# Performance work log

Hardware: AMD Instinct MI355X
Metric: run time of the kernel (lower is better)

The kernel has to match this reference:

```python
import jax, jax.numpy as jnp
import numpy as np

IN_DIM = 4096
OUT_DIM = 4096
CODEBOOK_SIZE = 65536
LAYER_ID = 3
HASH_A, HASH_B, HASH_C = 10007, 20011, 40009
SIGN_HASH_A, SIGN_HASH_B, SIGN_HASH_C = 4099, 6151, 14887
SIGNED_HASH = True
BATCH = 8192


def _hash_tables():
    i = jnp.arange(OUT_DIM, dtype=jnp.int64 if jax.config.jax_enable_x64 else jnp.int32)[:, None]
    j = jnp.arange(IN_DIM, dtype=i.dtype)[None, :]
    idx = (i * HASH_A + j * HASH_B + LAYER_ID * HASH_C) % CODEBOOK_SIZE
    bits = (i * SIGN_HASH_A + j * SIGN_HASH_B + LAYER_ID * SIGN_HASH_C) % 2
    signs = bits.astype(jnp.float32) * 2.0 - 1.0
    return idx, signs


def setup_inputs() -> dict:
    key = jax.random.key(0)
    kx, kc = jax.random.split(key)
    x = jax.random.normal(kx, (BATCH, IN_DIM), dtype=jnp.float32)
    codebook = jax.random.normal(kc, (CODEBOOK_SIZE,), dtype=jnp.float32) * 0.01
    bias = jnp.zeros((OUT_DIM,), dtype=jnp.float32)
    return {"x": x, "codebook": codebook, "bias": bias}


def reference(x, codebook, bias):
    idx, signs = _hash_tables()  # [out_dim, in_dim] each
    weight = codebook[idx]  # gather from tiny codebook -> [out_dim, in_dim]
    if SIGNED_HASH:
        weight = weight * signs.astype(weight.dtype)
    # F.linear: y = x @ W^T + b
    return jnp.einsum('bi,oi->bo', x, weight) + bias
```

## Files before the change

kernel.cpp:

```cpp
#include <hip/hip_runtime.h>
#include <hip/hip_bf16.h>

constexpr int M_ = 8192;
constexpr int N_ = 4096;
constexpr int K_ = 4096;
constexpr int CBOOK = 65536;
constexpr int HA = 10007, HB = 20011;
constexpr int HC3 = 3 * 40009;

constexpr int C0 = 197;

constexpr int BM = 256, BN = 256, BK = 32;
constexpr int NKT = K_ / BK;

using bf16x8 = __bf16 __attribute__((ext_vector_type(8)));
using f32x4  = float __attribute__((ext_vector_type(4)));
using u16x8  = unsigned short __attribute__((ext_vector_type(8)));

typedef __attribute__((address_space(3))) void lds_void_t;
typedef const __attribute__((address_space(1))) void gbl_void_t;

static __device__ __forceinline__ unsigned short f2bf(float f) {
    __bf16 h = (__bf16)f;
    return __builtin_bit_cast(unsigned short, h);
}

constexpr int P2N   = 8 * 65536;
constexpr int P2B   = P2N / 256;

__global__ __launch_bounds__(256) void prep_p2(const float* __restrict__ cb,
                                               unsigned short* __restrict__ P2p) {
    const int t = blockIdx.x * 256 + threadIdx.x;
    const int p = t >> 16;
    const int i = t & 65535;
    const int u = i + p;
    float v = cb[(u * HB + HC3) & (CBOOK - 1)];
    if (u & 1) v = -v;
    P2p[t] = f2bf(v);
}

constexpr int GENB  = N_ * K_ / 8 / 256;
constexpr int CONVB = M_ * K_ / 8 / 256;

__global__ __launch_bounds__(256) void prep_main(const float* __restrict__ x,
                                                 const unsigned short* __restrict__ P2p,
                                                 unsigned short* __restrict__ Wf,
                                                 unsigned short* __restrict__ xb) {
    const int b = blockIdx.x;
    if (b < GENB) {
        const int t    = b * 256 + threadIdx.x;
        const int slot = t & 1023;
        const int kt   = (t >> 10) & 127;
        const int nb   = t >> 17;
        const int row  = slot >> 2;
        const int key  = (row >> 1) & 3;
        const int n  = (nb << 8) + row;
        const int k0 = (kt << 5) + (((slot & 3) ^ key) << 3);
        const int u0 = (C0 * n + k0) & (CBOOK - 1);
        const u16x8 w = *reinterpret_cast<const u16x8*>(
            P2p + ((u0 & 7) << 16) + (u0 & 65528));
        *reinterpret_cast<u16x8*>(&Wf[(size_t)t * 8]) = w;
    } else {
        const size_t t = (size_t)(b - GENB) * 256 + threadIdx.x;
        const float4* p = reinterpret_cast<const float4*>(x) + t * 2;
        const float4 a = p[0], c = p[1];
        u16x8 out;
        out[0] = f2bf(a.x); out[1] = f2bf(a.y); out[2] = f2bf(a.z); out[3] = f2bf(a.w);
        out[4] = f2bf(c.x); out[5] = f2bf(c.y); out[6] = f2bf(c.z); out[7] = f2bf(c.w);
        reinterpret_cast<u16x8*>(xb)[t] = out;
    }
}

__global__ __launch_bounds__(512, 2) void gemm_kernel(
        const unsigned short* __restrict__ A,
        const unsigned short* __restrict__ Wf,
        const float* __restrict__ bias,
        float* __restrict__ C) {
    __shared__ __align__(16) unsigned short sm[3 * 8192 * 2];
    unsigned short* As = sm;
    unsigned short* Bs = sm + 3 * 8192;

    const int tid  = threadIdx.x;
    const int lane = tid & 63;
    const int w    = tid >> 6;
    const int wm   = w >> 2;
    const int wn   = w & 3;
    const int m0 = blockIdx.y * BM;
    const int n0 = blockIdx.x * BN;

    const int quad = lane >> 4;
    const int l16  = lane & 15;

    const int sblk = (lane & 3) ^ ((lane >> 3) & 3);
    const unsigned short* aLane =
        A + (size_t)(m0 + w * 16 + (lane >> 2)) * K_ + sblk * 8;
    const unsigned short* bLane =
        Wf + (size_t)blockIdx.x * NKT * 8192 + tid * 8;

    const int rblk = (quad ^ ((l16 >> 1) & 3)) * 8;
    const unsigned short* aRd = As + (wm * 128 + l16) * 32 + rblk;
    const unsigned short* bRd = Bs + (wn * 64 + l16) * 32 + rblk;

    f32x4 acc[8][4] = {};

    auto STAGE_HALF = [&](int kt, int bs, int r) {
        __builtin_amdgcn_global_load_lds(
            (gbl_void_t*)(aLane + (size_t)r * 128 * K_ + (size_t)kt * BK),
            (lds_void_t*)(As + bs * 8192 + (r * 512 + w * 64) * 8), 16, 0, 0);
        __builtin_amdgcn_global_load_lds(
            (gbl_void_t*)(bLane + (size_t)kt * 8192 + r * 4096),
            (lds_void_t*)(Bs + bs * 8192 + (r * 512 + w * 64) * 8), 16, 0, 0);
    };

    STAGE_HALF(0, 0, 0); STAGE_HALF(0, 0, 1);
    STAGE_HALF(1, 1, 0); STAGE_HALF(1, 1, 1);
    asm volatile("s_waitcnt vmcnt(4)" ::: "memory");
    __builtin_amdgcn_s_barrier();
    __builtin_amdgcn_sched_barrier(0);

    int bC = 0;
    for (int kt = 0; kt < NKT; ++kt) {
        int bS = bC + 2; if (bS >= 3) bS -= 3;
        const bool st = (kt + 2 < NKT);

        bf16x8 bfr[4], afr0[4];
#pragma unroll
        for (int nt = 0; nt < 4; ++nt)
            bfr[nt] = *reinterpret_cast<const bf16x8*>(bRd + bC * 8192 + nt * 512);
#pragma unroll
        for (int mt = 0; mt < 4; ++mt)
            afr0[mt] = *reinterpret_cast<const bf16x8*>(aRd + bC * 8192 + mt * 512);
        if (st) STAGE_HALF(kt + 2, bS, 0);
        __builtin_amdgcn_sched_barrier(0);
        __builtin_amdgcn_s_barrier();
        asm volatile("s_waitcnt lgkmcnt(0)" ::: "memory");
        __builtin_amdgcn_sched_barrier(0);
        __builtin_amdgcn_s_setprio(1);
#pragma unroll
        for (int mt = 0; mt < 4; ++mt)
#pragma unroll
            for (int nt = 0; nt < 4; ++nt)
                acc[mt][nt] = __builtin_amdgcn_mfma_f32_16x16x32_bf16(
                    afr0[mt], bfr[nt], acc[mt][nt], 0, 0, 0);
        __builtin_amdgcn_s_setprio(0);
        __builtin_amdgcn_sched_barrier(0);
        __builtin_amdgcn_s_barrier();
        __builtin_amdgcn_sched_barrier(0);

        bf16x8 afr1[4];
#pragma unroll
        for (int mt = 0; mt < 4; ++mt)
            afr1[mt] = *reinterpret_cast<const bf16x8*>(aRd + bC * 8192 + (mt + 4) * 512);
        if (st) STAGE_HALF(kt + 2, bS, 1);
        __builtin_amdgcn_sched_barrier(0);
        __builtin_amdgcn_s_barrier();
        asm volatile("s_waitcnt lgkmcnt(0)" ::: "memory");
        __builtin_amdgcn_sched_barrier(0);
        __builtin_amdgcn_s_setprio(1);
#pragma unroll
        for (int mt = 0; mt < 4; ++mt)
#pragma unroll
            for (int nt = 0; nt < 4; ++nt)
                acc[mt + 4][nt] = __builtin_amdgcn_mfma_f32_16x16x32_bf16(
                    afr1[mt], bfr[nt], acc[mt + 4][nt], 0, 0, 0);
        __builtin_amdgcn_s_setprio(0);
        __builtin_amdgcn_sched_barrier(0);

        if (kt < NKT - 1) {
            if (st) asm volatile("s_waitcnt vmcnt(4)" ::: "memory");
            else    asm volatile("s_waitcnt vmcnt(0)" ::: "memory");
            __builtin_amdgcn_s_barrier();
            __builtin_amdgcn_sched_barrier(0);
        }

        ++bC; if (bC == 3) bC = 0;
    }

#pragma unroll
    for (int nt = 0; nt < 4; ++nt) {
        const int col = n0 + wn * 64 + nt * 16 + l16;
        const float bv = bias[col];
#pragma unroll
        for (int mt = 0; mt < 8; ++mt) {
            const int rowb = m0 + wm * 128 + mt * 16 + quad * 4;
#pragma unroll
            for (int r = 0; r < 4; ++r)
                C[(size_t)(rowb + r) * N_ + col] = acc[mt][nt][r] + bv;
        }
    }
}

__global__ __launch_bounds__(256) void naive_kernel(const float* __restrict__ x,
                                                    const float* __restrict__ cb,
                                                    const float* __restrict__ bias,
                                                    float* __restrict__ out) {
    const size_t t = (size_t)blockIdx.x * 256 + threadIdx.x;
    const int row = (int)(t / N_);
    const int col = (int)(t % N_);
    float s = bias[col];
    const float* xr = x + (size_t)row * K_;
    const int h = col * HA + HC3;
    for (int i = 0; i < K_; ++i) {
        float v = cb[(h + i * HB) & (CBOOK - 1)];
        s += xr[i] * (((col ^ i) & 1) ? -v : v);
    }
    out[t] = s;
}

extern "C" void kernel_launch(void* const* d_in, const int* in_sizes, int n_in,
                              void* d_out, int out_size, void* d_ws, size_t ws_size,
                              hipStream_t stream) {
    const float* x    = (const float*)d_in[0];
    const float* cb   = (const float*)d_in[1];
    const float* bias = (const float*)d_in[2];
    float* out = (float*)d_out;

    const size_t wBytes = (size_t)N_ * K_ * sizeof(unsigned short);
    const size_t xBytes = (size_t)M_ * K_ * sizeof(unsigned short);
    const size_t pBytes = (size_t)P2N * sizeof(unsigned short);

    if (ws_size >= wBytes + xBytes + pBytes) {
        unsigned short* Wf  = (unsigned short*)d_ws;
        unsigned short* xb  = (unsigned short*)((char*)d_ws + wBytes);
        unsigned short* P2p = (unsigned short*)((char*)d_ws + wBytes + xBytes);
        prep_p2<<<P2B, 256, 0, stream>>>(cb, P2p);
        prep_main<<<GENB + CONVB, 256, 0, stream>>>(x, P2p, Wf, xb);
        gemm_kernel<<<dim3(N_ / BN, M_ / BM), 512, 0, stream>>>(xb, Wf, bias, out);
    } else {
        naive_kernel<<<(int)((size_t)M_ * N_ / 256), 256, 0, stream>>>(x, cb, bias, out);
    }
}
```

Measured before the change: 451.8 us.

## Deepen GEMM LDS pipeline to four stages with register-prefetched fragments

The GEMM main loop moves from a 3-buffer LDS ring with two half-iteration phases to a 4-buffer ring with prefetch distance 3. Each iteration now has a single barrier, issues the global-to-LDS loads for tile kt+3, runs all 32 MFMAs, and then reads the next tile's fragments into registers. This removes two barriers and two lgkmcnt waits per K step, and lets LDS reads for the next step overlap the current MFMAs. In exchange, LDS use rises to 128 KB per block and more fragment registers stay live, which raises register pressure.

Measured after the change: 451.0 us. No clear change (-0.2%).

```diff
diff --git a/kernel.cpp b/kernel.cpp
--- a/kernel.cpp
+++ b/kernel.cpp
@@ -76,9 +76,9 @@
         const unsigned short* __restrict__ Wf,
         const float* __restrict__ bias,
         float* __restrict__ C) {
-    __shared__ __align__(16) unsigned short sm[3 * 8192 * 2];
+    __shared__ __align__(16) unsigned short sm[4 * 8192 * 2];
     unsigned short* As = sm;
-    unsigned short* Bs = sm + 3 * 8192;
+    unsigned short* Bs = sm + 4 * 8192;
 
     const int tid  = threadIdx.x;
     const int lane = tid & 63;
@@ -102,78 +102,57 @@
     const unsigned short* bRd = Bs + (wn * 64 + l16) * 32 + rblk;
 
     f32x4 acc[8][4] = {};
-
-    auto STAGE_HALF = [&](int kt, int bs, int r) {
-        __builtin_amdgcn_global_load_lds(
-            (gbl_void_t*)(aLane + (size_t)r * 128 * K_ + (size_t)kt * BK),
-            (lds_void_t*)(As + bs * 8192 + (r * 512 + w * 64) * 8), 16, 0, 0);
-        __builtin_amdgcn_global_load_lds(
-            (gbl_void_t*)(bLane + (size_t)kt * 8192 + r * 4096),
-            (lds_void_t*)(Bs + bs * 8192 + (r * 512 + w * 64) * 8), 16, 0, 0);
+    bf16x8 bfr[4], afr[8];
+
+    auto STAGE = [&](int kt, int bs) {
+#pragma unroll
+        for (int r = 0; r < 2; ++r) {
+            __builtin_amdgcn_global_load_lds(
+                (gbl_void_t*)(aLane + (size_t)r * 128 * K_ + (size_t)kt * BK),
+                (lds_void_t*)(As + bs * 8192 + (r * 512 + w * 64) * 8), 16, 0, 0);
+            __builtin_amdgcn_global_load_lds(
+                (gbl_void_t*)(bLane + (size_t)kt * 8192 + r * 4096),
+                (lds_void_t*)(Bs + bs * 8192 + (r * 512 + w * 64) * 8), 16, 0, 0);
+        }
     };
-
-    STAGE_HALF(0, 0, 0); STAGE_HALF(0, 0, 1);
-    STAGE_HALF(1, 1, 0); STAGE_HALF(1, 1, 1);
-    asm volatile("s_waitcnt vmcnt(4)" ::: "memory");
+    auto READF = [&](int kt) {
+        const int bs = kt & 3;
+#pragma unroll
+        for (int nt = 0; nt < 4; ++nt)
+            bfr[nt] = *reinterpret_cast<const bf16x8*>(bRd + bs * 8192 + nt * 512);
+#pragma unroll
+        for (int mt = 0; mt < 8; ++mt)
+            afr[mt] = *reinterpret_cast<const bf16x8*>(aRd + bs * 8192 + mt * 512);
+    };
+
+    STAGE(0, 0); STAGE(1, 1); STAGE(2, 2);
+    asm volatile("s_waitcnt vmcnt(8)" ::: "memory");
     __builtin_amdgcn_s_barrier();
     __builtin_amdgcn_sched_barrier(0);
-
-    int bC = 0;
+    READF(0);
+    __builtin_amdgcn_sched_barrier(0);
+
     for (int kt = 0; kt < NKT; ++kt) {
-        int bS = bC + 2; if (bS >= 3) bS -= 3;
-        const bool st = (kt + 2 < NKT);
-
-        bf16x8 bfr[4], afr0[4];
-#pragma unroll
-        for (int nt = 0; nt < 4; ++nt)
-            bfr[nt] = *reinterpret_cast<const bf16x8*>(bRd + bC * 8192 + nt * 512);
-#pragma unroll
-        for (int mt = 0; mt < 4; ++mt)
-            afr0[mt] = *reinterpret_cast<const bf16x8*>(aRd + bC * 8192 + mt * 512);
-        if (st) STAGE_HALF(kt + 2, bS, 0);
-        __builtin_amdgcn_sched_barrier(0);
+        if (kt + 2 < NKT)      asm volatile("s_waitcnt vmcnt(4)" ::: "memory");
+        else if (kt + 1 < NKT) asm volatile("s_waitcnt vmcnt(0)" ::: "memory");
         __builtin_amdgcn_s_barrier();
-        asm volatile("s_waitcnt lgkmcnt(0)" ::: "memory");
-        __builtin_amdgcn_sched_barrier(0);
+        __builtin_amdgcn_sched_barrier(0);
+
+        if (kt + 3 < NKT) STAGE(kt + 3, (kt + 3) & 3);
+        __builtin_amdgcn_sched_barrier(0);
+
         __builtin_amdgcn_s_setprio(1);
 #pragma unroll
-        for (int mt = 0; mt < 4; ++mt)
+        for (int mt = 0; mt < 8; ++mt)
 #pragma unroll
             for (int nt = 0; nt < 4; ++nt)
                 acc[mt][nt] = __builtin_amdgcn_mfma_f32_16x16x32_bf16(
-                    afr0[mt], bfr[nt], acc[mt][nt], 0, 0, 0);
+                    afr[mt], bfr[nt], acc[mt][nt], 0, 0, 0);
         __builtin_amdgcn_s_setprio(0);
         __builtin_amdgcn_sched_barrier(0);
-        __builtin_amdgcn_s_barrier();
-        __builtin_amdgcn_sched_barrier(0);
-
-        bf16x8 afr1[4];
-#pragma unroll
-        for (int mt = 0; mt < 4; ++mt)
-            afr1[mt] = *reinterpret_cast<const bf16x8*>(aRd + bC * 8192 + (mt + 4) * 512);
-        if (st) STAGE_HALF(kt + 2, bS, 1);
-        __builtin_amdgcn_sched_barrier(0);
-        __builtin_amdgcn_s_barrier();
-        asm volatile("s_waitcnt lgkmcnt(0)" ::: "memory");
-        __builtin_amdgcn_sched_barrier(0);
-        __builtin_amdgcn_s_setprio(1);
-#pragma unroll
-        for (int mt = 0; mt < 4; ++mt)
-#pragma unroll
-            for (int nt = 0; nt < 4; ++nt)
-                acc[mt + 4][nt] = __builtin_amdgcn_mfma_f32_16x16x32_bf16(
-                    afr1[mt], bfr[nt], acc[mt + 4][nt], 0, 0, 0);
-        __builtin_amdgcn_s_setprio(0);
-        __builtin_amdgcn_sched_barrier(0);
-
-        if (kt < NKT - 1) {
-            if (st) asm volatile("s_waitcnt vmcnt(4)" ::: "memory");
-            else    asm volatile("s_waitcnt vmcnt(0)" ::: "memory");
-            __builtin_amdgcn_s_barrier();
-            __builtin_amdgcn_sched_barrier(0);
-        }
-
-        ++bC; if (bC == 3) bC = 0;
+
+        if (kt + 1 < NKT) READF(kt + 1);
+        __builtin_amdgcn_sched_barrier(0);
     }
 
 #pragma unroll
```
